# Optimization experiments

Hardware: AMD Instinct MI355X
Metric: run time of the kernel (lower is better)

Reference implementation:

```python
import jax, jax.numpy as jnp
import numpy as np
import math

MIN_NORM = 1e-15
EPS = 4e-3  # float32 boundary eps used by PoincareBall.proj
C = 1.0


def artanh(x):
    x = jnp.clip(x, -1.0 + 1e-7, 1.0 - 1e-7)
    return 0.5 * (jnp.log1p(x) - jnp.log1p(-x))


def _norm(x):
    return jnp.maximum(jnp.linalg.norm(x, axis=-1, keepdims=True), MIN_NORM)


def proj(x, c):
    n = _norm(x)
    maxnorm = (1.0 - EPS) / jnp.sqrt(c)
    return jnp.where(n > maxnorm, x / n * maxnorm, x)


def expmap0(u, c):
    sc = jnp.sqrt(c)
    n = _norm(u)
    return jnp.tanh(sc * n) * u / (sc * n)


def logmap0(p, c):
    sc = jnp.sqrt(c)
    n = _norm(p)
    return artanh(sc * n) * p / (sc * n)


def mobius_add(x, y, c):
    x2 = jnp.sum(x * x, -1, keepdims=True)
    y2 = jnp.sum(y * y, -1, keepdims=True)
    xy = jnp.sum(x * y, -1, keepdims=True)
    num = (1 + 2 * c * xy + c * y2) * x + (1 - c * x2) * y
    den = 1 + 2 * c * xy + c * c * x2 * y2
    return num / jnp.maximum(den, MIN_NORM)


def mobius_matvec(m, x, c):
    sc = jnp.sqrt(c)
    xn = _norm(x)
    mx = x @ m.T
    mxn = _norm(mx)
    res = jnp.tanh(mxn / xn * artanh(sc * xn)) * mx / (mxn * sc)
    zero = jnp.all(mx == 0, axis=-1, keepdims=True)
    return jnp.where(zero, jnp.zeros((), x.dtype), res)


def hnn_layer(x, W, b, c):
    # HypLinear (dropout=0, use_bias=1) followed by HypAct(relu); proj_tan0 is identity for PoincareBall.
    res = proj(mobius_matvec(W, x, c), c)
    hb = proj(expmap0(b.reshape(1, -1), c), c)
    res = proj(mobius_add(res, hb, c), c)
    xt = jax.nn.relu(logmap0(res, c))
    return proj(expmap0(xt, c), c)


def setup_inputs():
    key = jax.random.key(0)
    ks = jax.random.split(key, 5)
    B, N, K, D = 4, 2000, 5, 32
    H1, H2 = 160, 32  # H_layer1: 32 -> 32*5, H_layer2: 32 -> 32
    # points on the Poincare ball (small norm so logmap0 is well-conditioned)
    in_feats = 0.05 * jax.random.normal(ks[0], (B, N, D), jnp.float32)
    # one-hot neighbor adjacency [batch, agent, nei, agent]
    nei_idx = jax.random.randint(ks[1], (B, N, K), 0, N)
    in_nei = jax.nn.one_hot(nei_idx, N, dtype=jnp.float32)
    # xavier_uniform with gain sqrt(2), zero bias (reset_parameters)
    b1w = math.sqrt(2.0) * math.sqrt(6.0 / (H1 + D))
    b2w = math.sqrt(2.0) * math.sqrt(6.0 / (H2 + H2))
    W1 = jax.random.uniform(ks[2], (H1, D), jnp.float32, -b1w, b1w)
    W2 = jax.random.uniform(ks[3], (H2, H2), jnp.float32, -b2w, b2w)
    b1 = jnp.zeros((H1,), jnp.float32)
    b2 = jnp.zeros((H2,), jnp.float32)
    return {"in_feats": in_feats, "in_nei": in_nei, "W1": W1, "b1": b1,
            "W2": W2, "b2": b2, "h_dim": 32, "head": 5}


def reference(in_feats, in_nei, W1, b1, W2, b2, h_dim, head):
    c = C
    B, N, D = in_feats.shape
    K = in_nei.shape[2]
    # tangent-space features (proj_tan0 is identity)
    feats = logmap0(in_feats, c)                                   # [B,N,D]
    agent = proj(expmap0(feats[:, :, None, :], c), c)              # [B,N,1,D]
    # one-hot adjacency gather: equals matmul(in_nei, repeat(feats)) in the torch code
    nbr_t = jnp.einsum('bnkm,bmd->bnkd', in_nei, feats)            # [B,N,K,D]
    nbr = proj(expmap0(nbr_t, c), c)
    # query heads
    q = logmap0(hnn_layer(agent, W1, b1, c), c)                    # [B,N,1,h*head]
    q = q.reshape(B, N, 1, h_dim, head).transpose(0, 1, 4, 2, 3)   # [B,N,head,1,h]
    # key heads; the torch code recomputes H_layer1(neighbor_repr) for values with
    # identical weights/inputs (dropout=0), so values == keys and we reuse them.
    kv = logmap0(hnn_layer(nbr, W1, b1, c), c)
    kv = kv.reshape(B, N, K, h_dim, head).transpose(0, 1, 4, 2, 3)  # [B,N,head,K,h]
    att = jax.nn.softmax(jnp.einsum('bnhqd,bnhkd->bnhqk', q, kv), axis=-1)  # [B,N,head,1,K]
    att_record = att.reshape(B, N, head, K)
    out = jnp.einsum('bnhqk,bnhkd->bnhqd', att, kv).mean(axis=2)   # [B,N,1,h]
    out = out.reshape(B, N, h_dim)
    out = proj(expmap0(out, c), c)
    out = hnn_layer(out, W2, b2, c)                                # [B,N,32]
    return out, att_record
```

## Files before the change

### kernel.cpp

```cpp
#include <hip/hip_runtime.h>
#include <math.h>

#define BB 4
#define NN 2000
#define KK 5
#define DD 32
#define H1 160
#define HEAD 5
#define HDIM 32
#define MAXNORM 0.996f
#define MINN 1e-15f

#define NROWS (BB * NN * KK)
#define F4_PER_ROW (NN / 4)
#define G_BLOCKS 2000
#define SCAN_BLOCKS (NROWS / 4)

typedef float vfloat4 __attribute__((ext_vector_type(4)));

__device__ __forceinline__ float artanh_f(float x) {
    x = fminf(fmaxf(x, -1.0f + 1e-7f), 1.0f - 1e-7f);
    return 0.5f * (log1pf(x) - log1pf(-x));
}

__device__ __forceinline__ float wave_sum(float v) {
#pragma unroll
    for (int o = 32; o > 0; o >>= 1) v += __shfl_xor(v, o, 64);
    return v;
}

__device__ __forceinline__ float wave_sum32(float v) {
#pragma unroll
    for (int o = 16; o > 0; o >>= 1) v += __shfl_xor(v, o, 64);
    return v;
}

__global__ __launch_bounds__(256) void scan_kernel(const float* __restrict__ nei,
                                                   int* __restrict__ idx) {
    int lane = threadIdx.x & 63;
    int wave = (int)((blockIdx.x * 256u + threadIdx.x) >> 6);
    const vfloat4* __restrict__ row = (const vfloat4*)(nei + (size_t)wave * NN);
    int pos = -1;
    vfloat4 v[4];

#pragma unroll
    for (int j = 0; j < 4; ++j)
        v[j] = __builtin_nontemporal_load(row + (lane + 64 * j));
#pragma unroll
    for (int j = 0; j < 4; ++j) {
        int base = (lane + 64 * j) * 4;
        if (v[j][0] > 0.5f) pos = base;
        if (v[j][1] > 0.5f) pos = base + 1;
        if (v[j][2] > 0.5f) pos = base + 2;
        if (v[j][3] > 0.5f) pos = base + 3;
    }
    if (__ballot(pos >= 0) == 0ull) {
#pragma unroll
        for (int j = 0; j < 4; ++j) {
            int e = 256 + lane + 64 * j;
            if (e < F4_PER_ROW) {
                v[j] = __builtin_nontemporal_load(row + e);
            } else {
                vfloat4 z = {0.f, 0.f, 0.f, 0.f};
                v[j] = z;
            }
        }
#pragma unroll
        for (int j = 0; j < 4; ++j) {
            int base = (256 + lane + 64 * j) * 4;
            if (v[j][0] > 0.5f) pos = base;
            if (v[j][1] > 0.5f) pos = base + 1;
            if (v[j][2] > 0.5f) pos = base + 2;
            if (v[j][3] > 0.5f) pos = base + 3;
        }
    }
#pragma unroll
    for (int o = 32; o > 0; o >>= 1) pos = max(pos, __shfl_xor(pos, o, 64));
    if (lane == 0) idx[wave] = pos;
}

__global__ __launch_bounds__(256, 4) void g_kernel(const float* __restrict__ xin,
                                                   const float* __restrict__ W1,
                                                   const float* __restrict__ b1,
                                                   float* __restrict__ g) {
    int lane = threadIdx.x & 63;
    int wave = (int)blockIdx.x * 4 + (int)(threadIdx.x >> 6);
    bool j2ok = lane < (H1 - 128);

    float x = (lane < DD) ? xin[wave * DD + lane] : 0.f;

    float n = fmaxf(sqrtf(wave_sum(x * x)), MINN);
    float fa = artanh_f(n);
    float f = (fa / n) * x;
    float fn = fmaxf(fa, MINN);
    float tp = tanhf(fn);
    float p = (tp / fn) * f;
    float pn = tp;
    if (pn > MAXNORM) p *= MAXNORM / pn;
    float xn = fmaxf(fminf(pn, MAXNORM), MINN);

    float mx0 = 0.f, mx1 = 0.f, mx2 = 0.f;
#pragma unroll
    for (int d = 0; d < DD; ++d) {
        float pd = __shfl(p, d, 64);
        mx0 += W1[lane * DD + d] * pd;
        mx1 += W1[(lane + 64) * DD + d] * pd;
        if (j2ok) mx2 += W1[(lane + 128) * DD + d] * pd;
    }
    float m2 = mx0 * mx0 + mx1 * mx1 + (j2ok ? mx2 * mx2 : 0.f);
    float mxn = fmaxf(sqrtf(wave_sum(m2)), MINN);
    float tr = tanhf(mxn / xn * artanh_f(xn));
    float sc = tr / mxn;
    float r0 = sc * mx0, r1 = sc * mx1, r2 = sc * mx2;
    float rn = tr;
    if (rn > MAXNORM) { float s = MAXNORM / rn; r0 *= s; r1 *= s; r2 *= s; }
    rn = fminf(rn, MAXNORM);

    float bb0 = b1[lane], bb1 = b1[lane + 64], bb2 = j2ok ? b1[lane + 128] : 0.f;
    float bn = fmaxf(sqrtf(wave_sum(bb0 * bb0 + bb1 * bb1 + bb2 * bb2)), MINN);
    float tb = tanhf(bn);
    float bs = tb / bn;
    float h0 = bs * bb0, h1 = bs * bb1, h2 = bs * bb2;
    float hn = tb;
    if (hn > MAXNORM) { float s = MAXNORM / hn; h0 *= s; h1 *= s; h2 *= s; }
    hn = fminf(hn, MAXNORM);

    float x2s = rn * rn;
    float y2s = hn * hn;
    float xys = wave_sum(r0 * h0 + r1 * h1 + (j2ok ? r2 * h2 : 0.f));
    float ca = 1.f + 2.f * xys + y2s;
    float cb = 1.f - x2s;
    float den = fmaxf(1.f + 2.f * xys + x2s * y2s, MINN);
    float a0 = (ca * r0 + cb * h0) / den;
    float a1 = (ca * r1 + cb * h1) / den;
    float a2 = (ca * r2 + cb * h2) / den;
    float an = fmaxf(sqrtf(wave_sum(a0 * a0 + a1 * a1 + (j2ok ? a2 * a2 : 0.f))), MINN);
    if (an > MAXNORM) { float s = MAXNORM / an; a0 *= s; a1 *= s; a2 *= s; }
    float an2 = fmaxf(fminf(an, MAXNORM), MINN);

    float ls = artanh_f(an2) / an2;
    float t0 = fmaxf(ls * a0, 0.f), t1 = fmaxf(ls * a1, 0.f), t2 = fmaxf(ls * a2, 0.f);
    float tn = fmaxf(sqrtf(wave_sum(t0 * t0 + t1 * t1 + (j2ok ? t2 * t2 : 0.f))), MINN);
    float te = tanhf(tn);
    float es = te / tn;
    float y0 = es * t0, y1 = es * t1, y2 = es * t2;
    float yn = te;
    float s2 = (yn > MAXNORM) ? (MAXNORM / yn) : 1.f;
    y0 *= s2; y1 *= s2; y2 *= s2;
    float yn2 = fmaxf(fminf(yn, MAXNORM), MINN);
    float gs = artanh_f(yn2) / yn2;

    float* go = g + (size_t)wave * H1;
    go[lane] = gs * y0;
    go[lane + 64] = gs * y1;
    if (j2ok) go[lane + 128] = gs * y2;
}

__global__ __launch_bounds__(256, 4) void fused_att_out_kernel(const float* __restrict__ g,
                                                               const int* __restrict__ idx,
                                                               const float* __restrict__ W2,
                                                               const float* __restrict__ b2,
                                                               float* __restrict__ out,
                                                               float* __restrict__ att_out) {
    int wave = (blockIdx.x * blockDim.x + threadIdx.x) >> 6;
    int lane = threadIdx.x & 63;
    if (wave >= BB * NN) return;
    int r = wave;
    int b = r / NN;
    int d = lane & 31;

    const float* gq = g + (size_t)r * H1;
    float q[HEAD];
#pragma unroll
    for (int h = 0; h < HEAD; ++h) q[h] = gq[d * HEAD + h];

    int nb[KK];
#pragma unroll
    for (int k = 0; k < KK; ++k) nb[k] = idx[r * KK + k];
    float kv[KK][HEAD];
#pragma unroll
    for (int k = 0; k < KK; ++k) {
        const float* gk = g + (size_t)(b * NN + nb[k]) * H1 + d * HEAD;
#pragma unroll
        for (int h = 0; h < HEAD; ++h) kv[k][h] = gk[h];
    }
    float s[KK][HEAD];
#pragma unroll
    for (int k = 0; k < KK; ++k)
#pragma unroll
        for (int h = 0; h < HEAD; ++h) s[k][h] = wave_sum32(q[h] * kv[k][h]);

    float att[HEAD][KK];
#pragma unroll
    for (int h = 0; h < HEAD; ++h) {
        float mxv = s[0][h];
#pragma unroll
        for (int k = 1; k < KK; ++k) mxv = fmaxf(mxv, s[k][h]);
        float sum = 0.f;
#pragma unroll
        for (int k = 0; k < KK; ++k) { att[h][k] = expf(s[k][h] - mxv); sum += att[h][k]; }
        float inv = 1.f / sum;
#pragma unroll
        for (int k = 0; k < KK; ++k) att[h][k] *= inv;
    }
    if (lane < HEAD * KK) {
        int h = lane / KK, k = lane % KK;
        att_out[(size_t)r * HEAD * KK + lane] = att[h][k];
    }

    float o = 0.f;
#pragma unroll
    for (int h = 0; h < HEAD; ++h)
#pragma unroll
        for (int k = 0; k < KK; ++k) o += att[h][k] * kv[k][h];
    o *= (1.f / HEAD);

    float n = fmaxf(sqrtf(wave_sum32(o * o)), MINN);
    float to = tanhf(n);
    o *= to / n;
    float on = to;
    if (on > MAXNORM) o *= MAXNORM / on;
    float xn = fmaxf(fminf(on, MAXNORM), MINN);

    float mx = 0.f;
#pragma unroll
    for (int dd = 0; dd < HDIM; ++dd) {
        float od = __shfl(o, dd, 64);
        mx += W2[d * HDIM + dd] * od;
    }
    float mxn = fmaxf(sqrtf(wave_sum32(mx * mx)), MINN);
    float tr = tanhf(mxn / xn * artanh_f(xn));
    mx *= tr / mxn;
    float rn = tr;
    if (rn > MAXNORM) mx *= MAXNORM / rn;
    rn = fminf(rn, MAXNORM);

    float hb = b2[d];
    float bn = fmaxf(sqrtf(wave_sum32(hb * hb)), MINN);
    float tb = tanhf(bn);
    hb *= tb / bn;
    float hn = tb;
    if (hn > MAXNORM) hb *= MAXNORM / hn;
    hn = fminf(hn, MAXNORM);

    float x2s = rn * rn;
    float y2s = hn * hn;
    float xys = wave_sum32(mx * hb);
    float ca = 1.f + 2.f * xys + y2s;
    float cb = 1.f - x2s;
    float den = fmaxf(1.f + 2.f * xys + x2s * y2s, MINN);
    float a = (ca * mx + cb * hb) / den;
    float an = fmaxf(sqrtf(wave_sum32(a * a)), MINN);
    if (an > MAXNORM) a *= MAXNORM / an;
    float an2 = fmaxf(fminf(an, MAXNORM), MINN);

    a = fmaxf((artanh_f(an2) / an2) * a, 0.f);
    float tn = fmaxf(sqrtf(wave_sum32(a * a)), MINN);
    float te = tanhf(tn);
    a *= te / tn;
    float yn = te;
    if (yn > MAXNORM) a *= MAXNORM / yn;

    if (lane < HDIM) out[(size_t)r * HDIM + lane] = a;
}

extern "C" void kernel_launch(void* const* d_in, const int* in_sizes, int n_in,
                              void* d_out, int out_size, void* d_ws, size_t ws_size,
                              hipStream_t stream) {
    const float* in_feats = (const float*)d_in[0];
    const float* in_nei = (const float*)d_in[1];
    const float* W1 = (const float*)d_in[2];
    const float* b1 = (const float*)d_in[3];
    const float* W2 = (const float*)d_in[4];
    const float* b2 = (const float*)d_in[5];

    int* idx = (int*)d_ws;
    size_t idx_bytes = ((size_t)BB * NN * KK * sizeof(int) + 255) & ~(size_t)255;
    float* g = (float*)((char*)d_ws + idx_bytes);

    float* out = (float*)d_out;
    float* att = out + (size_t)BB * NN * HDIM;

    hipLaunchKernelGGL(g_kernel, dim3(G_BLOCKS), dim3(256), 0, stream,
                       in_feats, W1, b1, g);
    hipLaunchKernelGGL(scan_kernel, dim3(SCAN_BLOCKS), dim3(256), 0, stream,
                       in_nei, idx);
    hipLaunchKernelGGL(fused_att_out_kernel, dim3((BB * NN * 64 + 255) / 256), dim3(256), 0, stream,
                       g, idx, W2, b2, out, att);
}
```

Measured before the change: 504.8 us.

## Fuse one-hot neighbor scan into attention/output kernel, dropping idx buffer

Merges the adjacency scan into the attention kernel. Each wave now scans all five one-hot rows for its agent, packs the found indices into a 64-bit value and reduces it across lanes, so the separate scan launch and the idx round trip through memory are gone. The catch is that each wave now issues five rows of loads before its attention work, raising register pressure and possibly reducing memory-level parallelism. The launch_bounds occupancy hint is also dropped.

```diff
diff --git a/kernel.cpp b/kernel.cpp
--- a/kernel.cpp
+++ b/kernel.cpp
@@ -14,7 +14,7 @@
 #define NROWS (BB * NN * KK)
 #define F4_PER_ROW (NN / 4)
 #define G_BLOCKS 2000
-#define SCAN_BLOCKS (NROWS / 4)
+#define MEGA_BLOCKS 2000
 
 typedef float vfloat4 __attribute__((ext_vector_type(4)));
 
@@ -33,50 +33,6 @@
 #pragma unroll
     for (int o = 16; o > 0; o >>= 1) v += __shfl_xor(v, o, 64);
     return v;
-}
-
-__global__ __launch_bounds__(256) void scan_kernel(const float* __restrict__ nei,
-                                                   int* __restrict__ idx) {
-    int lane = threadIdx.x & 63;
-    int wave = (int)((blockIdx.x * 256u + threadIdx.x) >> 6);
-    const vfloat4* __restrict__ row = (const vfloat4*)(nei + (size_t)wave * NN);
-    int pos = -1;
-    vfloat4 v[4];
-
-#pragma unroll
-    for (int j = 0; j < 4; ++j)
-        v[j] = __builtin_nontemporal_load(row + (lane + 64 * j));
-#pragma unroll
-    for (int j = 0; j < 4; ++j) {
-        int base = (lane + 64 * j) * 4;
-        if (v[j][0] > 0.5f) pos = base;
-        if (v[j][1] > 0.5f) pos = base + 1;
-        if (v[j][2] > 0.5f) pos = base + 2;
-        if (v[j][3] > 0.5f) pos = base + 3;
-    }
-    if (__ballot(pos >= 0) == 0ull) {
-#pragma unroll
-        for (int j = 0; j < 4; ++j) {
-            int e = 256 + lane + 64 * j;
-            if (e < F4_PER_ROW) {
-                v[j] = __builtin_nontemporal_load(row + e);
-            } else {
-                vfloat4 z = {0.f, 0.f, 0.f, 0.f};
-                v[j] = z;
-            }
-        }
-#pragma unroll
-        for (int j = 0; j < 4; ++j) {
-            int base = (256 + lane + 64 * j) * 4;
-            if (v[j][0] > 0.5f) pos = base;
-            if (v[j][1] > 0.5f) pos = base + 1;
-            if (v[j][2] > 0.5f) pos = base + 2;
-            if (v[j][3] > 0.5f) pos = base + 3;
-        }
-    }
-#pragma unroll
-    for (int o = 32; o > 0; o >>= 1) pos = max(pos, __shfl_xor(pos, o, 64));
-    if (lane == 0) idx[wave] = pos;
 }
 
 __global__ __launch_bounds__(256, 4) void g_kernel(const float* __restrict__ xin,
@@ -156,27 +112,85 @@
     if (j2ok) go[lane + 128] = gs * y2;
 }
 
-__global__ __launch_bounds__(256, 4) void fused_att_out_kernel(const float* __restrict__ g,
-                                                               const int* __restrict__ idx,
-                                                               const float* __restrict__ W2,
-                                                               const float* __restrict__ b2,
-                                                               float* __restrict__ out,
-                                                               float* __restrict__ att_out) {
-    int wave = (blockIdx.x * blockDim.x + threadIdx.x) >> 6;
+__global__ __launch_bounds__(256) void scan_att_out_kernel(const float* __restrict__ nei,
+                                                           const float* __restrict__ g,
+                                                           const float* __restrict__ W2,
+                                                           const float* __restrict__ b2,
+                                                           float* __restrict__ out,
+                                                           float* __restrict__ att_out) {
     int lane = threadIdx.x & 63;
-    if (wave >= BB * NN) return;
-    int r = wave;
+    int r = (int)((blockIdx.x * 256u + threadIdx.x) >> 6);
     int b = r / NN;
+
+    int pos[KK];
+    {
+        const float* rows[KK];
+#pragma unroll
+        for (int k = 0; k < KK; ++k)
+            rows[k] = nei + (size_t)(r * KK + k) * NN;
+
+        vfloat4 v[KK][4];
+#pragma unroll
+        for (int k = 0; k < KK; ++k)
+#pragma unroll
+            for (int j = 0; j < 4; ++j)
+                v[k][j] = __builtin_nontemporal_load((const vfloat4*)rows[k] + (lane + 64 * j));
+#pragma unroll
+        for (int k = 0; k < KK; ++k) {
+            pos[k] = -1;
+#pragma unroll
+            for (int j = 0; j < 4; ++j) {
+                int base = (lane + 64 * j) * 4;
+                if (v[k][j][0] > 0.5f) pos[k] = base;
+                if (v[k][j][1] > 0.5f) pos[k] = base + 1;
+                if (v[k][j][2] > 0.5f) pos[k] = base + 2;
+                if (v[k][j][3] > 0.5f) pos[k] = base + 3;
+            }
+        }
+#pragma unroll
+        for (int k = 0; k < KK; ++k) {
+            if (__ballot(pos[k] >= 0) == 0ull) {
+                vfloat4 w[4];
+#pragma unroll
+                for (int j = 0; j < 4; ++j) {
+                    int e = 256 + lane + 64 * j;
+                    if (e < F4_PER_ROW) {
+                        w[j] = __builtin_nontemporal_load((const vfloat4*)rows[k] + e);
+                    } else {
+                        vfloat4 z = {0.f, 0.f, 0.f, 0.f};
+                        w[j] = z;
+                    }
+                }
+#pragma unroll
+                for (int j = 0; j < 4; ++j) {
+                    int base = (256 + lane + 64 * j) * 4;
+                    if (w[j][0] > 0.5f) pos[k] = base;
+                    if (w[j][1] > 0.5f) pos[k] = base + 1;
+                    if (w[j][2] > 0.5f) pos[k] = base + 2;
+                    if (w[j][3] > 0.5f) pos[k] = base + 3;
+                }
+            }
+        }
+    }
+    unsigned long long packed = 0ull;
+#pragma unroll
+    for (int k = 0; k < KK; ++k)
+        if (pos[k] >= 0)
+            packed |= (unsigned long long)(pos[k] + 1) << (12 * k);
+#pragma unroll
+    for (int o = 32; o > 0; o >>= 1) packed |= __shfl_xor(packed, o, 64);
+
+    int nb[KK];
+#pragma unroll
+    for (int k = 0; k < KK; ++k)
+        nb[k] = (int)((packed >> (12 * k)) & 0xFFFull) - 1;
+
     int d = lane & 31;
-
     const float* gq = g + (size_t)r * H1;
     float q[HEAD];
 #pragma unroll
     for (int h = 0; h < HEAD; ++h) q[h] = gq[d * HEAD + h];
 
-    int nb[KK];
-#pragma unroll
-    for (int k = 0; k < KK; ++k) nb[k] = idx[r * KK + k];
     float kv[KK][HEAD];
 #pragma unroll
     for (int k = 0; k < KK; ++k) {
@@ -274,17 +288,13 @@
     const float* W2 = (const float*)d_in[4];
     const float* b2 = (const float*)d_in[5];
 
-    int* idx = (int*)d_ws;
-    size_t idx_bytes = ((size_t)BB * NN * KK * sizeof(int) + 255) & ~(size_t)255;
-    float* g = (float*)((char*)d_ws + idx_bytes);
+    float* g = (float*)d_ws;
 
     float* out = (float*)d_out;
     float* att = out + (size_t)BB * NN * HDIM;
 
     hipLaunchKernelGGL(g_kernel, dim3(G_BLOCKS), dim3(256), 0, stream,
                        in_feats, W1, b1, g);
-    hipLaunchKernelGGL(scan_kernel, dim3(SCAN_BLOCKS), dim3(256), 0, stream,
-                       in_nei, idx);
-    hipLaunchKernelGGL(fused_att_out_kernel, dim3((BB * NN * 64 + 255) / 256), dim3(256), 0, stream,
-                       g, idx, W2, b2, out, att);
-}
+    hipLaunchKernelGGL(scan_att_out_kernel, dim3(MEGA_BLOCKS), dim3(256), 0, stream,
+                       in_nei, g, W2, b2, out, att);
+}
```

Result: no change. 503.7 us (-0.2%).
